# Optimization experiments

Hardware: AMD Instinct MI355X
Metric: run time of the kernel (lower is better)

The kernel has to match this reference:

```python
import jax, jax.numpy as jnp
import numpy as np

H = 16  # hidden/input size
EPS = 1e-5


def _lstm_layer(xs, W_ih, W_hh, b_ih, b_hh):
    """xs: [T, B, in]. Returns (ys [T,B,H], h_final [B,H]). PyTorch gate order i,f,g,o."""
    B = xs.shape[1]
    h0 = jnp.zeros((B, H), xs.dtype)
    c0 = jnp.zeros((B, H), xs.dtype)
    bias = b_ih + b_hh  # [4H]

    def step(carry, x_t):
        h, c = carry
        gates = x_t @ W_ih.T + h @ W_hh.T + bias  # [B, 4H]
        i, f, g, o = jnp.split(gates, 4, axis=-1)
        i = jax.nn.sigmoid(i)
        f = jax.nn.sigmoid(f)
        g = jnp.tanh(g)
        o = jax.nn.sigmoid(o)
        c = f * c + i * g
        h = o * jnp.tanh(c)
        return (h, c), h

    (h_fin, _), ys = jax.lax.scan(step, (h0, c0), xs)
    return ys, h_fin


def setup_inputs() -> dict:
    key = jax.random.key(0)
    ks = jax.random.split(key, 12)
    s = 1.0 / np.sqrt(H)  # PyTorch LSTM/Linear init scale
    B, T = 4096, 512
    x = jax.random.normal(ks[0], (B, T, H), dtype=jnp.float32)
    u = lambda k, shp: jax.random.uniform(k, shp, jnp.float32, -s, s)
    return {
        "x": x,
        "W_ih0": u(ks[1], (4 * H, H)), "W_hh0": u(ks[2], (4 * H, H)),
        "b_ih0": u(ks[3], (4 * H,)), "b_hh0": u(ks[4], (4 * H,)),
        "W_ih1": u(ks[5], (4 * H, H)), "W_hh1": u(ks[6], (4 * H, H)),
        "b_ih1": u(ks[7], (4 * H,)), "b_hh1": u(ks[8], (4 * H,)),
        "W_proj": u(ks[9], (H, H)), "b_proj": u(ks[10], (H,)),
        "ln_gamma": jnp.ones((H,), jnp.float32), "ln_beta": jnp.zeros((H,), jnp.float32),
    }


def reference(x, W_ih0, W_hh0, b_ih0, b_hh0, W_ih1, W_hh1, b_ih1, b_hh1,
              W_proj, b_proj, ln_gamma, ln_beta):
    xs = jnp.transpose(x, (1, 0, 2))  # [T, B, H] time-major for scan
    ys, _ = _lstm_layer(xs, W_ih0, W_hh0, b_ih0, b_hh0)
    _, h_n = _lstm_layer(ys, W_ih1, W_hh1, b_ih1, b_hh1)  # h_n[-1] == layer-2 final h
    z = h_n @ W_proj.T + b_proj  # [B, H]
    mu = jnp.mean(z, axis=-1, keepdims=True)
    var = jnp.mean(jnp.square(z - mu), axis=-1, keepdims=True)
    z = (z - mu) * jax.lax.rsqrt(var + EPS) * ln_gamma + ln_beta
    return jnp.tanh(z)
```

## Files before the change

kernel.cpp:

```cpp
#include <hip/hip_runtime.h>
#include <cstddef>

#define HH 16
#define TT 512
#define STG 16
#define NSTG (TT / STG)
#define LOG2E 1.44269504088896340736f

typedef float v2f __attribute__((ext_vector_type(2)));
typedef float v4f __attribute__((ext_vector_type(4)));

static __device__ __forceinline__ float fexp2(float x){ return __builtin_amdgcn_exp2f(x); }
static __device__ __forceinline__ float frcp (float x){ return __builtin_amdgcn_rcpf(x); }
static __device__ __forceinline__ float frsq (float x){ return __builtin_amdgcn_rsqf(x); }

static __device__ __forceinline__ float ftanh(float c){
    return frcp(1.0f + fexp2(c * (-2.0f*LOG2E))) * 2.0f - 1.0f;
}

#if __has_builtin(__builtin_amdgcn_mov_dpp)
template<int CTRL>
static __device__ __forceinline__ float qb(float v){
    return __builtin_bit_cast(float,
        __builtin_amdgcn_mov_dpp(__builtin_bit_cast(int,v), CTRL, 0xF, 0xF, true));
}
#else
template<int CTRL>
static __device__ __forceinline__ float qb(float v){
    return __builtin_bit_cast(float,
        __builtin_amdgcn_update_dpp(0, __builtin_bit_cast(int,v), CTRL, 0xF, 0xF, true));
}
#endif

static __device__ __forceinline__ v2f pkfma(v2f a, v2f b, v2f c){
    return __builtin_elementwise_fma(a, b, c);
}

static __device__ __forceinline__ void dot16_acc(const v4f* a, const v4f* w, v2f& s0, v2f& s1){
    s0 = pkfma(a[0].lo, w[0].lo, s0);  s1 = pkfma(a[0].hi, w[0].hi, s1);
    s0 = pkfma(a[1].lo, w[1].lo, s0);  s1 = pkfma(a[1].hi, w[1].hi, s1);
    s0 = pkfma(a[2].lo, w[2].lo, s0);  s1 = pkfma(a[2].hi, w[2].hi, s1);
    s0 = pkfma(a[3].lo, w[3].lo, s0);  s1 = pkfma(a[3].hi, w[3].hi, s1);
}

static __device__ __forceinline__ void dot16_first(const v4f* a, const v4f* w, v2f bias2,
                                                   v2f& s0, v2f& s1){
    s0 = pkfma(a[0].lo, w[0].lo, bias2);
    s1 = a[0].hi * w[0].hi;
    s0 = pkfma(a[1].lo, w[1].lo, s0);  s1 = pkfma(a[1].hi, w[1].hi, s1);
    s0 = pkfma(a[2].lo, w[2].lo, s0);  s1 = pkfma(a[2].hi, w[2].hi, s1);
    s0 = pkfma(a[3].lo, w[3].lo, s0);  s1 = pkfma(a[3].hi, w[3].hi, s1);
}

static __device__ __forceinline__ void ld4(v4f* dst, const float* p){
    const v4f* q = (const v4f*)p;
    dst[0] = q[0]; dst[1] = q[1]; dst[2] = q[2]; dst[3] = q[3];
}

__global__ __launch_bounds__(256, 4) void lstm_fused_kernel(
    const float* __restrict__ x,
    const float* __restrict__ W_ih0, const float* __restrict__ W_hh0,
    const float* __restrict__ b_ih0, const float* __restrict__ b_hh0,
    const float* __restrict__ W_ih1, const float* __restrict__ W_hh1,
    const float* __restrict__ b_ih1, const float* __restrict__ b_hh1,
    const float* __restrict__ W_proj, const float* __restrict__ b_proj,
    const float* __restrict__ ln_g, const float* __restrict__ ln_b,
    float* __restrict__ out)
{
    const int lane = threadIdx.x & 63;
    const int wave = threadIdx.x >> 6;
    const int b    = blockIdx.x * 4 + wave;

    const int g   = lane & 3;
    const int k   = lane >> 2;
    const int row = g * HH + k;

    __shared__ float sh[4 * 544];
    float* xb0 = sh + wave * 544;
    float* xb1 = xb0 + 256;
    float* h1w = xb1 + 256;
    float* h2w = h1w + 16;

    const bool  isg   = (g == 2);
    const float sc_in = isg ? (-2.0f * LOG2E) : (-LOG2E);

    v4f wih0[4], whh0[4], wih1[4], whh1[4];
#pragma unroll
    for (int q = 0; q < 4; ++q) {
        wih0[q] = ((const v4f*)(W_ih0 + row * HH))[q] * sc_in;
        whh0[q] = ((const v4f*)(W_hh0 + row * HH))[q] * sc_in;
        wih1[q] = ((const v4f*)(W_ih1 + row * HH))[q] * sc_in;
        whh1[q] = ((const v4f*)(W_hh1 + row * HH))[q] * sc_in;
    }
    const v2f bias0v = {(b_ih0[row] + b_hh0[row]) * sc_in, 0.f};
    const v2f bias1v = {(b_ih1[row] + b_hh1[row]) * sc_in, 0.f};

    const float* xg = x + (size_t)b * TT * HH;

    v4f xs = *(const v4f*)(xg + lane * 4);
    *(v4f*)(xb0 + lane * 4) = xs;
    xs = *(const v4f*)(xg + 256 + lane * 4);

    v4f xa[4];
    ld4(xa, xb0);

    float cs1, cs2 = 0.0f;
    v4f h1a[4], h2a[4];
#pragma unroll
    for (int q = 0; q < 4; ++q) h2a[q] = (v4f)(0.f);

    {
        v2f p0, p1;
        dot16_first(xa, wih0, bias0v, p0, p1);
        v2f ps = p0 + p1;
        float a1 = ps.x + ps.y;
        float r1 = frcp(1.0f + fexp2(a1));
        float i1 = qb<0x00>(r1), g1 = qb<0xAA>(r1), o1 = qb<0xFF>(r1);
        float gs1 = __builtin_fmaf(g1, -4.0f*LOG2E, 2.0f*LOG2E);
        cs1 = i1 * gs1;
        float h1n = o1 * (frcp(1.0f + fexp2(cs1)) * 2.0f - 1.0f);
        h1w[k] = h1n;
        ld4(h1a, h1w);
        ld4(xa, xb0 + HH);
    }

    for (int s = 0; s < NSTG; ++s) {
        float* cur = (s & 1) ? xb1 : xb0;
        float* nxt = (s & 1) ? xb0 : xb1;

        *(v4f*)(nxt + lane * 4) = xs;
        const int sp = (s + 2 < NSTG) ? (s + 2) : (NSTG - 1);
        xs = *(const v4f*)(xg + (size_t)sp * 256 + lane * 4);

#pragma unroll
        for (int ti = 0; ti < STG; ++ti) {
            __builtin_amdgcn_s_setprio(1);
            v2f p0, p1;
            dot16_first(xa, wih0, bias0v, p0, p1);
            dot16_acc(h1a, whh0, p0, p1);
            __builtin_amdgcn_s_setprio(0);
            v2f ps = p0 + p1;
            float a1 = ps.x + ps.y;
            float r1 = frcp(1.0f + fexp2(a1));
            float i1 = qb<0x00>(r1), f1 = qb<0x55>(r1);
            float g1 = qb<0xAA>(r1), o1 = qb<0xFF>(r1);
            float gs1 = __builtin_fmaf(g1, -4.0f*LOG2E, 2.0f*LOG2E);
            cs1 = __builtin_fmaf(f1, cs1, i1 * gs1);
            float h1n = o1 * (frcp(1.0f + fexp2(cs1)) * 2.0f - 1.0f);
            h1w[k] = h1n;

            __builtin_amdgcn_s_setprio(1);
            v2f q0, q1;
            dot16_first(h1a, wih1, bias1v, q0, q1);
            __builtin_amdgcn_s_setprio(0);

            ld4(h1a, h1w);
            ld4(xa, (ti <= 13) ? (cur + (ti + 2) * HH) : (nxt + (ti - 14) * HH));

            __builtin_amdgcn_s_setprio(1);
            dot16_acc(h2a, whh1, q0, q1);
            __builtin_amdgcn_s_setprio(0);
            v2f qs = q0 + q1;
            float a2 = qs.x + qs.y;
            float r2 = frcp(1.0f + fexp2(a2));
            float i2 = qb<0x00>(r2), f2 = qb<0x55>(r2);
            float g2 = qb<0xAA>(r2), o2 = qb<0xFF>(r2);
            float gs2 = __builtin_fmaf(g2, -4.0f*LOG2E, 2.0f*LOG2E);
            cs2 = __builtin_fmaf(f2, cs2, i2 * gs2);
            float h2n = o2 * (frcp(1.0f + fexp2(cs2)) * 2.0f - 1.0f);
            h2w[k] = h2n;
            ld4(h2a, h2w);
        }
    }

    const int u = lane & 15;
    v4f wp[4];
#pragma unroll
    for (int q = 0; q < 4; ++q) wp[q] = ((const v4f*)(W_proj + u * HH))[q];
    const v2f bpv = {b_proj[u], 0.f};
    v2f z0, z1;
    dot16_first(h2a, wp, bpv, z0, z1);
    v2f zs = z0 + z1;
    float z = zs.x + zs.y;

    float sacc = z;
    sacc += __shfl_xor(sacc, 1); sacc += __shfl_xor(sacc, 2);
    sacc += __shfl_xor(sacc, 4); sacc += __shfl_xor(sacc, 8);
    const float mu = sacc * (1.0f / 16.0f);

    const float d = z - mu;
    float q2 = d * d;
    q2 += __shfl_xor(q2, 1); q2 += __shfl_xor(q2, 2);
    q2 += __shfl_xor(q2, 4); q2 += __shfl_xor(q2, 8);
    const float var = q2 * (1.0f / 16.0f);

    const float rs  = frsq(var + 1e-5f);
    const float y   = d * rs * ln_g[u] + ln_b[u];
    const float res = ftanh(y);

    if (lane < 16) out[(size_t)b * HH + lane] = res;
}

extern "C" void kernel_launch(void* const* d_in, const int* in_sizes, int n_in,
                              void* d_out, int out_size, void* d_ws, size_t ws_size,
                              hipStream_t stream) {
    const float* x      = (const float*)d_in[0];
    const float* W_ih0  = (const float*)d_in[1];
    const float* W_hh0  = (const float*)d_in[2];
    const float* b_ih0  = (const float*)d_in[3];
    const float* b_hh0  = (const float*)d_in[4];
    const float* W_ih1  = (const float*)d_in[5];
    const float* W_hh1  = (const float*)d_in[6];
    const float* b_ih1  = (const float*)d_in[7];
    const float* b_hh1  = (const float*)d_in[8];
    const float* W_proj = (const float*)d_in[9];
    const float* b_proj = (const float*)d_in[10];
    const float* ln_g   = (const float*)d_in[11];
    const float* ln_b   = (const float*)d_in[12];
    float* out = (float*)d_out;

    const int B = in_sizes[0] / (TT * HH);
    dim3 grid(B / 4), block(256);
    hipLaunchKernelGGL(lstm_fused_kernel, grid, block, 0, stream,
                       x, W_ih0, W_hh0, b_ih0, b_hh0,
                       W_ih1, W_hh1, b_ih1, b_hh1,
                       W_proj, b_proj, ln_g, ln_b, out);
}
```

Baseline: 481.5 us.

## Load x via wave-uniform scalar loads instead of LDS double-buffer staging

Removes the per-wave LDS double buffer for the input sequence. It now reads each timestep's 16 inputs straight from global memory through a readfirstlane'd pointer, so the compiler can use scalar loads, with a two-step lookahead. It also flattens the staged loop into one loop unrolled by 8, drops the s_setprio hints, and shrinks shared memory to the h1/h2 exchange buffers. The aim is to cut LDS traffic and staging stores, at the risk of exposed scalar-load latency and SGPR operand constraints on the packed FMAs.

```diff
diff --git a/kernel.cpp b/kernel.cpp
--- a/kernel.cpp
+++ b/kernel.cpp
@@ -1,10 +1,9 @@
 #include <hip/hip_runtime.h>
 #include <cstddef>
+#include <cstdint>
 
 #define HH 16
 #define TT 512
-#define STG 16
-#define NSTG (TT / STG)
 #define LOG2E 1.44269504088896340736f
 
 typedef float v2f __attribute__((ext_vector_type(2)));
@@ -55,6 +54,13 @@
 static __device__ __forceinline__ void ld4(v4f* dst, const float* p){
     const v4f* q = (const v4f*)p;
     dst[0] = q[0]; dst[1] = q[1]; dst[2] = q[2]; dst[3] = q[3];
+}
+
+static __device__ __forceinline__ const float* uniform_ptr(const float* p){
+    uint64_t v = (uint64_t)p;
+    uint32_t lo = __builtin_amdgcn_readfirstlane((uint32_t)v);
+    uint32_t hi = __builtin_amdgcn_readfirstlane((uint32_t)(v >> 32));
+    return (const float*)(((uint64_t)hi << 32) | (uint64_t)lo);
 }
 
 __global__ __launch_bounds__(256, 4) void lstm_fused_kernel(
@@ -75,11 +81,9 @@
     const int k   = lane >> 2;
     const int row = g * HH + k;
 
-    __shared__ float sh[4 * 544];
-    float* xb0 = sh + wave * 544;
-    float* xb1 = xb0 + 256;
-    float* h1w = xb1 + 256;
-    float* h2w = h1w + 16;
+    __shared__ float sh[4 * 64];
+    float* h1w = sh + wave * 64;
+    float* h2w = h1w + 32;
 
     const bool  isg   = (g == 2);
     const float sc_in = isg ? (-2.0f * LOG2E) : (-LOG2E);
@@ -95,14 +99,10 @@
     const v2f bias0v = {(b_ih0[row] + b_hh0[row]) * sc_in, 0.f};
     const v2f bias1v = {(b_ih1[row] + b_hh1[row]) * sc_in, 0.f};
 
-    const float* xg = x + (size_t)b * TT * HH;
-
-    v4f xs = *(const v4f*)(xg + lane * 4);
-    *(v4f*)(xb0 + lane * 4) = xs;
-    xs = *(const v4f*)(xg + 256 + lane * 4);
+    const float* xg = uniform_ptr(x + (size_t)b * TT * HH);
 
     v4f xa[4];
-    ld4(xa, xb0);
+    ld4(xa, xg);
 
     float cs1, cs2 = 0.0f;
     v4f h1a[4], h2a[4];
@@ -121,56 +121,42 @@
         float h1n = o1 * (frcp(1.0f + fexp2(cs1)) * 2.0f - 1.0f);
         h1w[k] = h1n;
         ld4(h1a, h1w);
-        ld4(xa, xb0 + HH);
+        ld4(xa, xg + HH);
     }
 
-    for (int s = 0; s < NSTG; ++s) {
-        float* cur = (s & 1) ? xb1 : xb0;
-        float* nxt = (s & 1) ? xb0 : xb1;
-
-        *(v4f*)(nxt + lane * 4) = xs;
-        const int sp = (s + 2 < NSTG) ? (s + 2) : (NSTG - 1);
-        xs = *(const v4f*)(xg + (size_t)sp * 256 + lane * 4);
-
-#pragma unroll
-        for (int ti = 0; ti < STG; ++ti) {
-            __builtin_amdgcn_s_setprio(1);
-            v2f p0, p1;
-            dot16_first(xa, wih0, bias0v, p0, p1);
-            dot16_acc(h1a, whh0, p0, p1);
-            __builtin_amdgcn_s_setprio(0);
-            v2f ps = p0 + p1;
-            float a1 = ps.x + ps.y;
-            float r1 = frcp(1.0f + fexp2(a1));
-            float i1 = qb<0x00>(r1), f1 = qb<0x55>(r1);
-            float g1 = qb<0xAA>(r1), o1 = qb<0xFF>(r1);
-            float gs1 = __builtin_fmaf(g1, -4.0f*LOG2E, 2.0f*LOG2E);
-            cs1 = __builtin_fmaf(f1, cs1, i1 * gs1);
-            float h1n = o1 * (frcp(1.0f + fexp2(cs1)) * 2.0f - 1.0f);
-            h1w[k] = h1n;
-
-            __builtin_amdgcn_s_setprio(1);
-            v2f q0, q1;
-            dot16_first(h1a, wih1, bias1v, q0, q1);
-            __builtin_amdgcn_s_setprio(0);
-
-            ld4(h1a, h1w);
-            ld4(xa, (ti <= 13) ? (cur + (ti + 2) * HH) : (nxt + (ti - 14) * HH));
-
-            __builtin_amdgcn_s_setprio(1);
-            dot16_acc(h2a, whh1, q0, q1);
-            __builtin_amdgcn_s_setprio(0);
-            v2f qs = q0 + q1;
-            float a2 = qs.x + qs.y;
-            float r2 = frcp(1.0f + fexp2(a2));
-            float i2 = qb<0x00>(r2), f2 = qb<0x55>(r2);
-            float g2 = qb<0xAA>(r2), o2 = qb<0xFF>(r2);
-            float gs2 = __builtin_fmaf(g2, -4.0f*LOG2E, 2.0f*LOG2E);
-            cs2 = __builtin_fmaf(f2, cs2, i2 * gs2);
-            float h2n = o2 * (frcp(1.0f + fexp2(cs2)) * 2.0f - 1.0f);
-            h2w[k] = h2n;
-            ld4(h2a, h2w);
-        }
+#pragma unroll 8
+    for (int j = 0; j < TT; ++j) {
+        v2f p0, p1;
+        dot16_first(xa, wih0, bias0v, p0, p1);
+        dot16_acc(h1a, whh0, p0, p1);
+        v2f ps = p0 + p1;
+        float a1 = ps.x + ps.y;
+        float r1 = frcp(1.0f + fexp2(a1));
+        float i1 = qb<0x00>(r1), f1 = qb<0x55>(r1);
+        float g1 = qb<0xAA>(r1), o1 = qb<0xFF>(r1);
+        float gs1 = __builtin_fmaf(g1, -4.0f*LOG2E, 2.0f*LOG2E);
+        cs1 = __builtin_fmaf(f1, cs1, i1 * gs1);
+        float h1n = o1 * (frcp(1.0f + fexp2(cs1)) * 2.0f - 1.0f);
+        h1w[k] = h1n;
+
+        v2f q0, q1;
+        dot16_first(h1a, wih1, bias1v, q0, q1);
+
+        ld4(h1a, h1w);
+        const int jn = (j + 2 < TT) ? (j + 2) : (TT - 1);
+        ld4(xa, xg + jn * HH);
+
+        dot16_acc(h2a, whh1, q0, q1);
+        v2f qs = q0 + q1;
+        float a2 = qs.x + qs.y;
+        float r2 = frcp(1.0f + fexp2(a2));
+        float i2 = qb<0x00>(r2), f2 = qb<0x55>(r2);
+        float g2 = qb<0xAA>(r2), o2 = qb<0xFF>(r2);
+        float gs2 = __builtin_fmaf(g2, -4.0f*LOG2E, 2.0f*LOG2E);
+        cs2 = __builtin_fmaf(f2, cs2, i2 * gs2);
+        float h2n = o2 * (frcp(1.0f + fexp2(cs2)) * 2.0f - 1.0f);
+        h2w[k] = h2n;
+        ld4(h2a, h2w);
     }
 
     const int u = lane & 15;
```

New measurement: 558.7 us. 16.0% more time.
